# Performance work log

Measured on AMD Instinct MI355X. Metric: run time of the kernel, lower is better.

## Reference

```python
import jax, jax.numpy as jnp
import numpy as np

E, H, I, T, K = 8, 2048, 768, 1024, 2


def setup_inputs() -> dict:
    key = jax.random.key(0)
    k1, k2, k3, k4, k5 = jax.random.split(key, 5)
    hidden_states = jax.random.normal(k1, (T, H), jnp.float32)
    routing_weights = jax.random.uniform(k2, (T, K), jnp.float32)
    selected_experts = jax.random.randint(k3, (T, K), 0, E, jnp.int32)
    gate_up_proj = jax.random.normal(k4, (E, H, 2 * I), jnp.float32) * 0.02
    down_proj = jax.random.normal(k5, (E, I, H), jnp.float32) * 0.02
    return {
        "hidden_states": hidden_states,
        "routing_weights": routing_weights,
        "gate_up_proj": gate_up_proj,
        "down_proj": down_proj,
        "selected_experts": selected_experts,
    }


def _grouped_gemm(x, w, expert_ids):
    # x: [N, k], w: [E, k, d], expert_ids: [N] (sorted by expert).
    # Dense-masked grouped GEMM: accumulate each expert's masked matmul.
    n = x.shape[0]
    acc0 = jnp.zeros((n, w.shape[-1]), x.dtype)

    def step(acc, ew):
        e, we = ew
        xm = jnp.where((expert_ids == e)[:, None], x, jnp.zeros((), x.dtype))
        return acc + xm @ we, None

    acc, _ = jax.lax.scan(step, acc0, (jnp.arange(w.shape[0]), w))
    return acc


def reference(hidden_states, routing_weights, gate_up_proj, down_proj, selected_experts):
    t, h = hidden_states.shape
    k = selected_experts.shape[1]
    flat = selected_experts.reshape(-1)                     # [T*K]
    sort_idx = jnp.argsort(flat)                            # stable sort by expert id (permute)
    token_idx = sort_idx // k                               # source token per permuted row
    permuted = hidden_states[token_idx]                     # [T*K, H]
    experts_sorted = flat[sort_idx]                         # [T*K]

    fc1 = _grouped_gemm(permuted, gate_up_proj, experts_sorted)   # [T*K, 2I]
    a, b = jnp.split(fc1, 2, axis=-1)
    act = jax.nn.silu(a) * b                                # npu_swiglu
    fc2 = _grouped_gemm(act, down_proj, experts_sorted)     # [T*K, H]

    inv = jnp.argsort(sort_idx)                             # unpermute map (row_ids_map)
    unperm = fc2[inv].reshape(t, k, h)                      # [T, K, H]
    return jnp.einsum('tkh,tk->th', unperm, routing_weights)
```

## Files before the change

kernel.cpp:

```cpp
#include <hip/hip_runtime.h>
#include <math.h>

#define E_  8
#define H_  2048
#define I_  768
#define T_  1024
#define K_  2
#define TK_ 2048
#define GU_ 1536

typedef short  short8 __attribute__((ext_vector_type(8)));
typedef __bf16 bf16x8 __attribute__((ext_vector_type(8)));
typedef float  f32x4  __attribute__((ext_vector_type(4)));

static __device__ __forceinline__ short f2bf(float f) {
  union { float f; unsigned u; } v; v.f = f;
  unsigned r = (v.u + 0x7fffu + ((v.u >> 16) & 1u)) >> 16;
  return (short)r;
}

static __device__ __forceinline__ unsigned pk2bf(float a, float b) {
  unsigned ua = __float_as_uint(a) + 0x8000u;
  unsigned ub = __float_as_uint(b) + 0x8000u;
  return __builtin_amdgcn_perm(ub, ua, 0x07060302u);
}

#define GLOAD_LDS16(g, l)                                                   \
  __builtin_amdgcn_global_load_lds(                                         \
      (const __attribute__((address_space(1))) void*)(g),                   \
      (__attribute__((address_space(3))) void*)(l), 16, 0, 0)

#define MFMA_BF16_16x16x32 __builtin_amdgcn_mfma_f32_16x16x32_bf16

static __device__ __forceinline__ bf16x8 frag_ld(const unsigned short* base,
                                                 int row, int oct) {
  return *(const bf16x8*)(base + row * 64 + ((oct ^ (row & 7)) * 8));
}

static __device__ __forceinline__ bf16x8 bfrag_ld(const unsigned short* base,
                                                  int n, int o) {
  const unsigned short* p = base + n * 68 + o * 8;
  uint2 lo = *(const uint2*)p;
  uint2 hi = *(const uint2*)(p + 4);
  union { uint4 u; bf16x8 v; } c;
  c.u = make_uint4(lo.x, lo.y, hi.x, hi.y);
  return c.v;
}

__global__ __launch_bounds__(256) void prep_kernel(
    const float* __restrict__ X, unsigned short* __restrict__ Xb,
    float* __restrict__ out,
    const int* __restrict__ sel, int* __restrict__ offs,
    int* __restrict__ rows) {
  __shared__ int cnt[E_], cur[E_], loff[E_ + 1];
  if (blockIdx.x < 2048) {
    int i = blockIdx.x * 256 + threadIdx.x;
    float4 v = ((const float4*)X)[i];
    unsigned p0 = pk2bf(v.x, v.y), p1 = pk2bf(v.z, v.w);
    ((uint2*)Xb)[i] = make_uint2(p0, p1);
    ((float4*)out)[i] = make_float4(0.f, 0.f, 0.f, 0.f);
    return;
  }
  int t = threadIdx.x;
  if (t < E_) { cnt[t] = 0; cur[t] = 0; }
  __syncthreads();
  for (int p = t; p < TK_; p += 256) atomicAdd(&cnt[sel[p]], 1);
  __syncthreads();
  if (t == 0) {
    int s = 0;
    for (int e = 0; e < E_; ++e) { loff[e] = s; s += cnt[e]; }
    loff[E_] = s;
  }
  __syncthreads();
  if (t <= E_) offs[t] = loff[t];
  for (int p = t; p < TK_; p += 256) {
    int e = sel[p];
    int pos = loff[e] + atomicAdd(&cur[e], 1);
    rows[pos] = p;
  }
}

__global__ __launch_bounds__(256) void fc1_mfma(
    const unsigned short* __restrict__ Xb, const float* __restrict__ GUP,
    const int* __restrict__ offs, const int* __restrict__ rows,
    unsigned short* __restrict__ act) {
  __shared__ __align__(16) unsigned short As[2][128 * 64];
  __shared__ __align__(16) unsigned short Bs[2][64 * 68];

  int e    = blockIdx.y >> 4;
  int rbeg = offs[e], rend = offs[e + 1];
  int row0 = rbeg + (blockIdx.y & 15) * 128;
  if (row0 >= rend) return;
  int c0 = blockIdx.x * 32;

  int tid = threadIdx.x, lane = tid & 63, w = tid >> 6;
  int rl  = lane >> 3;
  int oct = (lane & 7) ^ rl;

  const unsigned short* agp[4];
#pragma unroll
  for (int i = 0; i < 4; ++i) {
    int arow = row0 + w * 32 + i * 8 + rl;
    int aidx = arow < rend ? arow : rend - 1;
    agp[i] = Xb + (size_t)(rows[aidx] >> 1) * H_ + oct * 8;
  }
  auto issueA = [&](int buf, int k0) {
#pragma unroll
    for (int i = 0; i < 4; ++i)
      GLOAD_LDS16(agp[i] + k0, &As[buf][0] + (w * 32 + i * 8) * 64);
  };

  int kt = tid >> 4, nt = tid & 15;
  int gbase = (nt < 8) ? (c0 + nt * 4) : (I_ + c0 + (nt - 8) * 4);
  const float* gupe = GUP + (size_t)e * H_ * GU_ + gbase;

  float4 vb[4];
  auto loadB = [&](int k0) {
#pragma unroll
    for (int i = 0; i < 4; ++i)
      vb[i] = *(const float4*)(gupe + (size_t)(k0 + kt * 4 + i) * GU_);
  };
  auto writeB = [&](int buf) {
#pragma unroll
    for (int j = 0; j < 4; ++j) {
      int n = nt * 4 + j;
      unsigned u0 = pk2bf(((const float*)&vb[0])[j], ((const float*)&vb[1])[j]);
      unsigned u1 = pk2bf(((const float*)&vb[2])[j], ((const float*)&vb[3])[j]);
      *(uint2*)(&Bs[buf][0] + n * 68 + kt * 4) = make_uint2(u0, u1);
    }
  };

  int m = lane & 15, qf = lane >> 4;
  f32x4 acc[2][4] = {};

  issueA(0, 0);
  loadB(0);
  writeB(0);
  int cur = 0;
  const int niter = H_ / 64;
#pragma unroll 1
  for (int it = 0; it < niter; ++it) {
    __syncthreads();
    if (it + 1 < niter) { issueA(cur ^ 1, (it + 1) * 64); loadB((it + 1) * 64); }
    const unsigned short* a_ = &As[cur][0];
    const unsigned short* b_ = &Bs[cur][0];
#pragma unroll
    for (int kk = 0; kk < 2; ++kk) {
      int o = kk * 4 + qf;
      bf16x8 af0 = frag_ld(a_, w * 32 + m,      o);
      bf16x8 af1 = frag_ld(a_, w * 32 + 16 + m, o);
      bf16x8 b0  = bfrag_ld(b_, m,      o);
      bf16x8 b1  = bfrag_ld(b_, 16 + m, o);
      bf16x8 b2  = bfrag_ld(b_, 32 + m, o);
      bf16x8 b3  = bfrag_ld(b_, 48 + m, o);
      acc[0][0] = MFMA_BF16_16x16x32(af0, b0, acc[0][0], 0, 0, 0);
      acc[0][1] = MFMA_BF16_16x16x32(af0, b1, acc[0][1], 0, 0, 0);
      acc[0][2] = MFMA_BF16_16x16x32(af0, b2, acc[0][2], 0, 0, 0);
      acc[0][3] = MFMA_BF16_16x16x32(af0, b3, acc[0][3], 0, 0, 0);
      acc[1][0] = MFMA_BF16_16x16x32(af1, b0, acc[1][0], 0, 0, 0);
      acc[1][1] = MFMA_BF16_16x16x32(af1, b1, acc[1][1], 0, 0, 0);
      acc[1][2] = MFMA_BF16_16x16x32(af1, b2, acc[1][2], 0, 0, 0);
      acc[1][3] = MFMA_BF16_16x16x32(af1, b3, acc[1][3], 0, 0, 0);
    }
    if (it + 1 < niter) writeB(cur ^ 1);
    cur ^= 1;
  }

#pragma unroll
  for (int mt = 0; mt < 2; ++mt)
#pragma unroll
    for (int g = 0; g < 2; ++g)
#pragma unroll
      for (int r = 0; r < 4; ++r) {
        int prow = row0 + w * 32 + mt * 16 + qf * 4 + r;
        if (prow < rend) {
          float gv = acc[mt][g][r], uv = acc[mt][g + 2][r];
          float a = gv / (1.0f + __expf(-gv)) * uv;
          act[(size_t)prow * I_ + c0 + g * 16 + m] = (unsigned short)f2bf(a);
        }
      }
}

__global__ __launch_bounds__(256) void fc2_mfma(
    const unsigned short* __restrict__ act, const float* __restrict__ DWN,
    const float* __restrict__ RW,
    const int* __restrict__ offs, const int* __restrict__ rows,
    float* __restrict__ out) {
  __shared__ __align__(16) unsigned short As[2][128 * 64];
  __shared__ __align__(16) unsigned short Bs[2][64 * 68];

  int e    = blockIdx.y >> 4;
  int rbeg = offs[e], rend = offs[e + 1];
  int row0 = rbeg + (blockIdx.y & 15) * 128;
  if (row0 >= rend) return;
  int c0 = blockIdx.x * 64;

  int tid = threadIdx.x, lane = tid & 63, w = tid >> 6;
  int rl  = lane >> 3;
  int oct = (lane & 7) ^ rl;

  const unsigned short* agp[4];
#pragma unroll
  for (int i = 0; i < 4; ++i) {
    int arow = row0 + w * 32 + i * 8 + rl;
    int aidx = arow < rend ? arow : rend - 1;
    agp[i] = act + (size_t)aidx * I_ + oct * 8;
  }
  auto issueA = [&](int buf, int k0) {
#pragma unroll
    for (int i = 0; i < 4; ++i)
      GLOAD_LDS16(agp[i] + k0, &As[buf][0] + (w * 32 + i * 8) * 64);
  };

  int kt = tid >> 4, nt = tid & 15;
  const float* dwe = DWN + (size_t)e * I_ * H_ + c0 + nt * 4;

  float4 vb[4];
  auto loadB = [&](int k0) {
#pragma unroll
    for (int i = 0; i < 4; ++i)
      vb[i] = *(const float4*)(dwe + (size_t)(k0 + kt * 4 + i) * H_);
  };
  auto writeB = [&](int buf) {
#pragma unroll
    for (int j = 0; j < 4; ++j) {
      int n = nt * 4 + j;
      unsigned u0 = pk2bf(((const float*)&vb[0])[j], ((const float*)&vb[1])[j]);
      unsigned u1 = pk2bf(((const float*)&vb[2])[j], ((const float*)&vb[3])[j]);
      *(uint2*)(&Bs[buf][0] + n * 68 + kt * 4) = make_uint2(u0, u1);
    }
  };

  int m = lane & 15, qf = lane >> 4;
  f32x4 acc[2][4] = {};

  issueA(0, 0);
  loadB(0);
  writeB(0);
  int cur = 0;
  const int niter = I_ / 64;
#pragma unroll 1
  for (int it = 0; it < niter; ++it) {
    __syncthreads();
    if (it + 1 < niter) { issueA(cur ^ 1, (it + 1) * 64); loadB((it + 1) * 64); }
    const unsigned short* a_ = &As[cur][0];
    const unsigned short* b_ = &Bs[cur][0];
#pragma unroll
    for (int kk = 0; kk < 2; ++kk) {
      int o = kk * 4 + qf;
      bf16x8 af0 = frag_ld(a_, w * 32 + m,      o);
      bf16x8 af1 = frag_ld(a_, w * 32 + 16 + m, o);
      bf16x8 b0  = bfrag_ld(b_, m,      o);
      bf16x8 b1  = bfrag_ld(b_, 16 + m, o);
      bf16x8 b2  = bfrag_ld(b_, 32 + m, o);
      bf16x8 b3  = bfrag_ld(b_, 48 + m, o);
      acc[0][0] = MFMA_BF16_16x16x32(af0, b0, acc[0][0], 0, 0, 0);
      acc[0][1] = MFMA_BF16_16x16x32(af0, b1, acc[0][1], 0, 0, 0);
      acc[0][2] = MFMA_BF16_16x16x32(af0, b2, acc[0][2], 0, 0, 0);
      acc[0][3] = MFMA_BF16_16x16x32(af0, b3, acc[0][3], 0, 0, 0);
      acc[1][0] = MFMA_BF16_16x16x32(af1, b0, acc[1][0], 0, 0, 0);
      acc[1][1] = MFMA_BF16_16x16x32(af1, b1, acc[1][1], 0, 0, 0);
      acc[1][2] = MFMA_BF16_16x16x32(af1, b2, acc[1][2], 0, 0, 0);
      acc[1][3] = MFMA_BF16_16x16x32(af1, b3, acc[1][3], 0, 0, 0);
    }
    if (it + 1 < niter) writeB(cur ^ 1);
    cur ^= 1;
  }

#pragma unroll
  for (int mt = 0; mt < 2; ++mt)
#pragma unroll
    for (int r = 0; r < 4; ++r) {
      int prow = row0 + w * 32 + mt * 16 + qf * 4 + r;
      if (prow < rend) {
        int pair = rows[prow];
        float rw = RW[pair];
        float* orow = out + (size_t)(pair >> 1) * H_ + c0 + m;
#pragma unroll
        for (int ntile = 0; ntile < 4; ++ntile)
          atomicAdd(orow + ntile * 16, rw * acc[mt][ntile][r]);
      }
    }
}

extern "C" void kernel_launch(void* const* d_in, const int* in_sizes, int n_in,
                              void* d_out, int out_size, void* d_ws, size_t ws_size,
                              hipStream_t stream) {
  const float* X   = (const float*)d_in[0];
  const float* RW  = (const float*)d_in[1];
  const float* GUP = (const float*)d_in[2];
  const float* DWN = (const float*)d_in[3];
  const int*   SEL = (const int*)d_in[4];
  float* out = (float*)d_out;

  char* ws = (char*)d_ws;
  int* offs = (int*)ws;
  int* rows = (int*)(ws + 1024);
  unsigned short* Xb  = (unsigned short*)(ws + 16384);
  unsigned short* act = (unsigned short*)(ws + 16384 + 4194304);

  hipLaunchKernelGGL(prep_kernel, dim3(2049), dim3(256), 0, stream,
                     X, Xb, out, SEL, offs, rows);
  hipLaunchKernelGGL(fc1_mfma, dim3(24, 128), dim3(256), 0, stream,
                     Xb, GUP, offs, rows, act);
  hipLaunchKernelGGL(fc2_mfma, dim3(32, 128), dim3(256), 0, stream,
                     act, DWN, RW, offs, rows, out);
}
```

Measured before the change: 252.9 us.

## Halve GEMM N-tile, swizzle B in LDS, raise occupancy in expert MFMA kernels

```diff
diff --git a/kernel.cpp b/kernel.cpp
--- a/kernel.cpp
+++ b/kernel.cpp
@@ -35,16 +35,6 @@
 static __device__ __forceinline__ bf16x8 frag_ld(const unsigned short* base,
                                                  int row, int oct) {
   return *(const bf16x8*)(base + row * 64 + ((oct ^ (row & 7)) * 8));
-}
-
-static __device__ __forceinline__ bf16x8 bfrag_ld(const unsigned short* base,
-                                                  int n, int o) {
-  const unsigned short* p = base + n * 68 + o * 8;
-  uint2 lo = *(const uint2*)p;
-  uint2 hi = *(const uint2*)(p + 4);
-  union { uint4 u; bf16x8 v; } c;
-  c.u = make_uint4(lo.x, lo.y, hi.x, hi.y);
-  return c.v;
 }
 
 __global__ __launch_bounds__(256) void prep_kernel(
@@ -80,18 +70,18 @@
   }
 }
 
-__global__ __launch_bounds__(256) void fc1_mfma(
+__global__ __launch_bounds__(256, 4) void fc1_mfma(
     const unsigned short* __restrict__ Xb, const float* __restrict__ GUP,
     const int* __restrict__ offs, const int* __restrict__ rows,
     unsigned short* __restrict__ act) {
   __shared__ __align__(16) unsigned short As[2][128 * 64];
-  __shared__ __align__(16) unsigned short Bs[2][64 * 68];
+  __shared__ __align__(16) unsigned short Bs[2][32 * 64];
 
   int e    = blockIdx.y >> 4;
   int rbeg = offs[e], rend = offs[e + 1];
   int row0 = rbeg + (blockIdx.y & 15) * 128;
   if (row0 >= rend) return;
-  int c0 = blockIdx.x * 32;
+  int c0 = blockIdx.x * 16;
 
   int tid = threadIdx.x, lane = tid & 63, w = tid >> 6;
   int rl  = lane >> 3;
@@ -110,28 +100,28 @@
       GLOAD_LDS16(agp[i] + k0, &As[buf][0] + (w * 32 + i * 8) * 64);
   };
 
-  int kt = tid >> 4, nt = tid & 15;
-  int gbase = (nt < 8) ? (c0 + nt * 4) : (I_ + c0 + (nt - 8) * 4);
-  const float* gupe = GUP + (size_t)e * H_ * GU_ + gbase;
-
-  float4 vb[4];
+  int q = tid & 7, kt2 = tid >> 3;
+  int gcol = (q < 4) ? (c0 + q * 4) : (I_ + c0 + (q - 4) * 4);
+  const float* gupe = GUP + (size_t)e * H_ * GU_ + gcol;
+
+  float4 vb[2];
   auto loadB = [&](int k0) {
 #pragma unroll
-    for (int i = 0; i < 4; ++i)
-      vb[i] = *(const float4*)(gupe + (size_t)(k0 + kt * 4 + i) * GU_);
+    for (int i = 0; i < 2; ++i)
+      vb[i] = *(const float4*)(gupe + (size_t)(k0 + kt2 * 2 + i) * GU_);
   };
   auto writeB = [&](int buf) {
 #pragma unroll
     for (int j = 0; j < 4; ++j) {
-      int n = nt * 4 + j;
-      unsigned u0 = pk2bf(((const float*)&vb[0])[j], ((const float*)&vb[1])[j]);
-      unsigned u1 = pk2bf(((const float*)&vb[2])[j], ((const float*)&vb[3])[j]);
-      *(uint2*)(&Bs[buf][0] + n * 68 + kt * 4) = make_uint2(u0, u1);
+      int n = q * 4 + j;
+      unsigned u = pk2bf(((const float*)&vb[0])[j], ((const float*)&vb[1])[j]);
+      int sw = (kt2 >> 2) ^ (n & 7);
+      *(unsigned*)(&Bs[buf][0] + n * 64 + sw * 8 + ((kt2 * 2) & 7)) = u;
     }
   };
 
   int m = lane & 15, qf = lane >> 4;
-  f32x4 acc[2][4] = {};
+  f32x4 acc[2][2] = {};
 
   issueA(0, 0);
   loadB(0);
@@ -149,18 +139,12 @@
       int o = kk * 4 + qf;
       bf16x8 af0 = frag_ld(a_, w * 32 + m,      o);
       bf16x8 af1 = frag_ld(a_, w * 32 + 16 + m, o);
-      bf16x8 b0  = bfrag_ld(b_, m,      o);
-      bf16x8 b1  = bfrag_ld(b_, 16 + m, o);
-      bf16x8 b2  = bfrag_ld(b_, 32 + m, o);
-      bf16x8 b3  = bfrag_ld(b_, 48 + m, o);
+      bf16x8 b0  = frag_ld(b_, m,      o);
+      bf16x8 b1  = frag_ld(b_, 16 + m, o);
       acc[0][0] = MFMA_BF16_16x16x32(af0, b0, acc[0][0], 0, 0, 0);
       acc[0][1] = MFMA_BF16_16x16x32(af0, b1, acc[0][1], 0, 0, 0);
-      acc[0][2] = MFMA_BF16_16x16x32(af0, b2, acc[0][2], 0, 0, 0);
-      acc[0][3] = MFMA_BF16_16x16x32(af0, b3, acc[0][3], 0, 0, 0);
       acc[1][0] = MFMA_BF16_16x16x32(af1, b0, acc[1][0], 0, 0, 0);
       acc[1][1] = MFMA_BF16_16x16x32(af1, b1, acc[1][1], 0, 0, 0);
-      acc[1][2] = MFMA_BF16_16x16x32(af1, b2, acc[1][2], 0, 0, 0);
-      acc[1][3] = MFMA_BF16_16x16x32(af1, b3, acc[1][3], 0, 0, 0);
     }
     if (it + 1 < niter) writeB(cur ^ 1);
     cur ^= 1;
@@ -169,31 +153,29 @@
 #pragma unroll
   for (int mt = 0; mt < 2; ++mt)
 #pragma unroll
-    for (int g = 0; g < 2; ++g)
-#pragma unroll
-      for (int r = 0; r < 4; ++r) {
-        int prow = row0 + w * 32 + mt * 16 + qf * 4 + r;
-        if (prow < rend) {
-          float gv = acc[mt][g][r], uv = acc[mt][g + 2][r];
-          float a = gv / (1.0f + __expf(-gv)) * uv;
-          act[(size_t)prow * I_ + c0 + g * 16 + m] = (unsigned short)f2bf(a);
-        }
+    for (int r = 0; r < 4; ++r) {
+      int prow = row0 + w * 32 + mt * 16 + qf * 4 + r;
+      if (prow < rend) {
+        float gv = acc[mt][0][r], uv = acc[mt][1][r];
+        float a = gv / (1.0f + __expf(-gv)) * uv;
+        act[(size_t)prow * I_ + c0 + m] = (unsigned short)f2bf(a);
       }
-}
-
-__global__ __launch_bounds__(256) void fc2_mfma(
+    }
+}
+
+__global__ __launch_bounds__(256, 4) void fc2_mfma(
     const unsigned short* __restrict__ act, const float* __restrict__ DWN,
     const float* __restrict__ RW,
     const int* __restrict__ offs, const int* __restrict__ rows,
     float* __restrict__ out) {
   __shared__ __align__(16) unsigned short As[2][128 * 64];
-  __shared__ __align__(16) unsigned short Bs[2][64 * 68];
+  __shared__ __align__(16) unsigned short Bs[2][32 * 64];
 
   int e    = blockIdx.y >> 4;
   int rbeg = offs[e], rend = offs[e + 1];
   int row0 = rbeg + (blockIdx.y & 15) * 128;
   if (row0 >= rend) return;
-  int c0 = blockIdx.x * 64;
+  int c0 = blockIdx.x * 32;
 
   int tid = threadIdx.x, lane = tid & 63, w = tid >> 6;
   int rl  = lane >> 3;
@@ -212,27 +194,27 @@
       GLOAD_LDS16(agp[i] + k0, &As[buf][0] + (w * 32 + i * 8) * 64);
   };
 
-  int kt = tid >> 4, nt = tid & 15;
-  const float* dwe = DWN + (size_t)e * I_ * H_ + c0 + nt * 4;
-
-  float4 vb[4];
+  int q = tid & 7, kt2 = tid >> 3;
+  const float* dwe = DWN + (size_t)e * I_ * H_ + c0 + q * 4;
+
+  float4 vb[2];
   auto loadB = [&](int k0) {
 #pragma unroll
-    for (int i = 0; i < 4; ++i)
-      vb[i] = *(const float4*)(dwe + (size_t)(k0 + kt * 4 + i) * H_);
+    for (int i = 0; i < 2; ++i)
+      vb[i] = *(const float4*)(dwe + (size_t)(k0 + kt2 * 2 + i) * H_);
   };
   auto writeB = [&](int buf) {
 #pragma unroll
     for (int j = 0; j < 4; ++j) {
-      int n = nt * 4 + j;
-      unsigned u0 = pk2bf(((const float*)&vb[0])[j], ((const float*)&vb[1])[j]);
-      unsigned u1 = pk2bf(((const float*)&vb[2])[j], ((const float*)&vb[3])[j]);
-      *(uint2*)(&Bs[buf][0] + n * 68 + kt * 4) = make_uint2(u0, u1);
+      int n = q * 4 + j;
+      unsigned u = pk2bf(((const float*)&vb[0])[j], ((const float*)&vb[1])[j]);
+      int sw = (kt2 >> 2) ^ (n & 7);
+      *(unsigned*)(&Bs[buf][0] + n * 64 + sw * 8 + ((kt2 * 2) & 7)) = u;
     }
   };
 
   int m = lane & 15, qf = lane >> 4;
-  f32x4 acc[2][4] = {};
+  f32x4 acc[2][2] = {};
 
   issueA(0, 0);
   loadB(0);
@@ -250,18 +232,12 @@
       int o = kk * 4 + qf;
       bf16x8 af0 = frag_ld(a_, w * 32 + m,      o);
       bf16x8 af1 = frag_ld(a_, w * 32 + 16 + m, o);
-      bf16x8 b0  = bfrag_ld(b_, m,      o);
-      bf16x8 b1  = bfrag_ld(b_, 16 + m, o);
-      bf16x8 b2  = bfrag_ld(b_, 32 + m, o);
-      bf16x8 b3  = bfrag_ld(b_, 48 + m, o);
+      bf16x8 b0  = frag_ld(b_, m,      o);
+      bf16x8 b1  = frag_ld(b_, 16 + m, o);
       acc[0][0] = MFMA_BF16_16x16x32(af0, b0, acc[0][0], 0, 0, 0);
       acc[0][1] = MFMA_BF16_16x16x32(af0, b1, acc[0][1], 0, 0, 0);
-      acc[0][2] = MFMA_BF16_16x16x32(af0, b2, acc[0][2], 0, 0, 0);
-      acc[0][3] = MFMA_BF16_16x16x32(af0, b3, acc[0][3], 0, 0, 0);
       acc[1][0] = MFMA_BF16_16x16x32(af1, b0, acc[1][0], 0, 0, 0);
       acc[1][1] = MFMA_BF16_16x16x32(af1, b1, acc[1][1], 0, 0, 0);
-      acc[1][2] = MFMA_BF16_16x16x32(af1, b2, acc[1][2], 0, 0, 0);
-      acc[1][3] = MFMA_BF16_16x16x32(af1, b3, acc[1][3], 0, 0, 0);
     }
     if (it + 1 < niter) writeB(cur ^ 1);
     cur ^= 1;
@@ -276,9 +252,8 @@
         int pair = rows[prow];
         float rw = RW[pair];
         float* orow = out + (size_t)(pair >> 1) * H_ + c0 + m;
-#pragma unroll
-        for (int ntile = 0; ntile < 4; ++ntile)
-          atomicAdd(orow + ntile * 16, rw * acc[mt][ntile][r]);
+        atomicAdd(orow,      rw * acc[mt][0][r]);
+        atomicAdd(orow + 16, rw * acc[mt][1][r]);
       }
     }
 }
@@ -301,8 +276,8 @@
 
   hipLaunchKernelGGL(prep_kernel, dim3(2049), dim3(256), 0, stream,
                      X, Xb, out, SEL, offs, rows);
-  hipLaunchKernelGGL(fc1_mfma, dim3(24, 128), dim3(256), 0, stream,
+  hipLaunchKernelGGL(fc1_mfma, dim3(48, 128), dim3(256), 0, stream,
                      Xb, GUP, offs, rows, act);
-  hipLaunchKernelGGL(fc2_mfma, dim3(32, 128), dim3(256), 0, stream,
+  hipLaunchKernelGGL(fc2_mfma, dim3(64, 128), dim3(256), 0, stream,
                      act, DWN, RW, offs, rows, out);
 }
```

New measurement: 280.5 us. +10.9%, slower.

## Deepen B prefetch to two stages, swizzle B LDS layout, hand-schedule waits

Applied to the files above, without the earlier changes.

```diff
diff --git a/kernel.cpp b/kernel.cpp
--- a/kernel.cpp
+++ b/kernel.cpp
@@ -9,7 +9,6 @@
 #define TK_ 2048
 #define GU_ 1536
 
-typedef short  short8 __attribute__((ext_vector_type(8)));
 typedef __bf16 bf16x8 __attribute__((ext_vector_type(8)));
 typedef float  f32x4  __attribute__((ext_vector_type(4)));
 
@@ -37,15 +36,41 @@
   return *(const bf16x8*)(base + row * 64 + ((oct ^ (row & 7)) * 8));
 }
 
-static __device__ __forceinline__ bf16x8 bfrag_ld(const unsigned short* base,
-                                                  int n, int o) {
-  const unsigned short* p = base + n * 68 + o * 8;
-  uint2 lo = *(const uint2*)p;
-  uint2 hi = *(const uint2*)(p + 4);
-  union { uint4 u; bf16x8 v; } c;
-  c.u = make_uint4(lo.x, lo.y, hi.x, hi.y);
-  return c.v;
-}
+#define STEP(IT, VC, VN)                                                    \
+  do {                                                                      \
+    asm volatile("s_waitcnt vmcnt(4)" ::: "memory");                        \
+    __builtin_amdgcn_s_barrier();                                           \
+    __builtin_amdgcn_sched_barrier(0);                                      \
+    int k1_ = ((IT) + 1 < niter ? (IT) + 1 : niter - 1) * 64;               \
+    int k2_ = ((IT) + 2 < niter ? (IT) + 2 : niter - 1) * 64;               \
+    issueA(cur ^ 1, k1_);                                                   \
+    __builtin_amdgcn_sched_barrier(0);                                      \
+    loadB(VN, k2_);                                                         \
+    const unsigned short* a_ = &As[cur][0];                                 \
+    const unsigned short* b_ = &Bs[cur][0];                                 \
+    _Pragma("unroll")                                                       \
+    for (int kk = 0; kk < 2; ++kk) {                                        \
+      int o = kk * 4 + qf;                                                  \
+      bf16x8 af0 = frag_ld(a_, w * 32 + m,      o);                         \
+      bf16x8 af1 = frag_ld(a_, w * 32 + 16 + m, o);                         \
+      bf16x8 b0  = frag_ld(b_, m,      o);                                  \
+      bf16x8 b1  = frag_ld(b_, 16 + m, o);                                  \
+      bf16x8 b2  = frag_ld(b_, 32 + m, o);                                  \
+      bf16x8 b3  = frag_ld(b_, 48 + m, o);                                  \
+      acc[0][0] = MFMA_BF16_16x16x32(af0, b0, acc[0][0], 0, 0, 0);          \
+      acc[0][1] = MFMA_BF16_16x16x32(af0, b1, acc[0][1], 0, 0, 0);          \
+      acc[0][2] = MFMA_BF16_16x16x32(af0, b2, acc[0][2], 0, 0, 0);          \
+      acc[0][3] = MFMA_BF16_16x16x32(af0, b3, acc[0][3], 0, 0, 0);          \
+      acc[1][0] = MFMA_BF16_16x16x32(af1, b0, acc[1][0], 0, 0, 0);          \
+      acc[1][1] = MFMA_BF16_16x16x32(af1, b1, acc[1][1], 0, 0, 0);          \
+      acc[1][2] = MFMA_BF16_16x16x32(af1, b2, acc[1][2], 0, 0, 0);          \
+      acc[1][3] = MFMA_BF16_16x16x32(af1, b3, acc[1][3], 0, 0, 0);          \
+    }                                                                       \
+    writeB(cur ^ 1, VC);                                                    \
+    asm volatile("s_waitcnt lgkmcnt(0)" ::: "memory");                      \
+    __builtin_amdgcn_sched_barrier(0);                                      \
+    cur ^= 1;                                                               \
+  } while (0)
 
 __global__ __launch_bounds__(256) void prep_kernel(
     const float* __restrict__ X, unsigned short* __restrict__ Xb,
@@ -80,12 +105,12 @@
   }
 }
 
-__global__ __launch_bounds__(256) void fc1_mfma(
+__global__ __launch_bounds__(256, 3) void fc1_mfma(
     const unsigned short* __restrict__ Xb, const float* __restrict__ GUP,
     const int* __restrict__ offs, const int* __restrict__ rows,
     unsigned short* __restrict__ act) {
   __shared__ __align__(16) unsigned short As[2][128 * 64];
-  __shared__ __align__(16) unsigned short Bs[2][64 * 68];
+  __shared__ __align__(16) unsigned short Bs[2][64 * 64];
 
   int e    = blockIdx.y >> 4;
   int rbeg = offs[e], rend = offs[e + 1];
@@ -114,56 +139,41 @@
   int gbase = (nt < 8) ? (c0 + nt * 4) : (I_ + c0 + (nt - 8) * 4);
   const float* gupe = GUP + (size_t)e * H_ * GU_ + gbase;
 
-  float4 vb[4];
-  auto loadB = [&](int k0) {
+  auto loadB = [&](float4 (&vb)[4], int k0) {
 #pragma unroll
     for (int i = 0; i < 4; ++i)
       vb[i] = *(const float4*)(gupe + (size_t)(k0 + kt * 4 + i) * GU_);
   };
-  auto writeB = [&](int buf) {
+  auto writeB = [&](int buf, const float4 (&vb)[4]) {
 #pragma unroll
     for (int j = 0; j < 4; ++j) {
       int n = nt * 4 + j;
       unsigned u0 = pk2bf(((const float*)&vb[0])[j], ((const float*)&vb[1])[j]);
       unsigned u1 = pk2bf(((const float*)&vb[2])[j], ((const float*)&vb[3])[j]);
-      *(uint2*)(&Bs[buf][0] + n * 68 + kt * 4) = make_uint2(u0, u1);
+      int phys = (kt >> 1) ^ (n & 7);
+      *(uint2*)(&Bs[buf][0] + n * 64 + phys * 8 + (kt & 1) * 4) =
+          make_uint2(u0, u1);
     }
   };
 
   int m = lane & 15, qf = lane >> 4;
   f32x4 acc[2][4] = {};
+  float4 vbA[4], vbB[4];
 
   issueA(0, 0);
-  loadB(0);
-  writeB(0);
+  __builtin_amdgcn_sched_barrier(0);
+  loadB(vbB, 0);
+  writeB(0, vbB);
+  loadB(vbA, 64);
+  asm volatile("s_waitcnt lgkmcnt(0)" ::: "memory");
+  __builtin_amdgcn_sched_barrier(0);
+
+  const int niter = H_ / 64;
   int cur = 0;
-  const int niter = H_ / 64;
 #pragma unroll 1
-  for (int it = 0; it < niter; ++it) {
-    __syncthreads();
-    if (it + 1 < niter) { issueA(cur ^ 1, (it + 1) * 64); loadB((it + 1) * 64); }
-    const unsigned short* a_ = &As[cur][0];
-    const unsigned short* b_ = &Bs[cur][0];
-#pragma unroll
-    for (int kk = 0; kk < 2; ++kk) {
-      int o = kk * 4 + qf;
-      bf16x8 af0 = frag_ld(a_, w * 32 + m,      o);
-      bf16x8 af1 = frag_ld(a_, w * 32 + 16 + m, o);
-      bf16x8 b0  = bfrag_ld(b_, m,      o);
-      bf16x8 b1  = bfrag_ld(b_, 16 + m, o);
-      bf16x8 b2  = bfrag_ld(b_, 32 + m, o);
-      bf16x8 b3  = bfrag_ld(b_, 48 + m, o);
-      acc[0][0] = MFMA_BF16_16x16x32(af0, b0, acc[0][0], 0, 0, 0);
-      acc[0][1] = MFMA_BF16_16x16x32(af0, b1, acc[0][1], 0, 0, 0);
-      acc[0][2] = MFMA_BF16_16x16x32(af0, b2, acc[0][2], 0, 0, 0);
-      acc[0][3] = MFMA_BF16_16x16x32(af0, b3, acc[0][3], 0, 0, 0);
-      acc[1][0] = MFMA_BF16_16x16x32(af1, b0, acc[1][0], 0, 0, 0);
-      acc[1][1] = MFMA_BF16_16x16x32(af1, b1, acc[1][1], 0, 0, 0);
-      acc[1][2] = MFMA_BF16_16x16x32(af1, b2, acc[1][2], 0, 0, 0);
-      acc[1][3] = MFMA_BF16_16x16x32(af1, b3, acc[1][3], 0, 0, 0);
-    }
-    if (it + 1 < niter) writeB(cur ^ 1);
-    cur ^= 1;
+  for (int it = 0; it < niter; it += 2) {
+    STEP(it,     vbA, vbB);
+    STEP(it + 1, vbB, vbA);
   }
 
 #pragma unroll
@@ -181,13 +191,13 @@
       }
 }
 
-__global__ __launch_bounds__(256) void fc2_mfma(
+__global__ __launch_bounds__(256, 3) void fc2_mfma(
     const unsigned short* __restrict__ act, const float* __restrict__ DWN,
     const float* __restrict__ RW,
     const int* __restrict__ offs, const int* __restrict__ rows,
     float* __restrict__ out) {
   __shared__ __align__(16) unsigned short As[2][128 * 64];
-  __shared__ __align__(16) unsigned short Bs[2][64 * 68];
+  __shared__ __align__(16) unsigned short Bs[2][64 * 64];
 
   int e    = blockIdx.y >> 4;
   int rbeg = offs[e], rend = offs[e + 1];
@@ -215,56 +225,41 @@
   int kt = tid >> 4, nt = tid & 15;
   const float* dwe = DWN + (size_t)e * I_ * H_ + c0 + nt * 4;
 
-  float4 vb[4];
-  auto loadB = [&](int k0) {
+  auto loadB = [&](float4 (&vb)[4], int k0) {
 #pragma unroll
     for (int i = 0; i < 4; ++i)
       vb[i] = *(const float4*)(dwe + (size_t)(k0 + kt * 4 + i) * H_);
   };
-  auto writeB = [&](int buf) {
+  auto writeB = [&](int buf, const float4 (&vb)[4]) {
 #pragma unroll
     for (int j = 0; j < 4; ++j) {
       int n = nt * 4 + j;
       unsigned u0 = pk2bf(((const float*)&vb[0])[j], ((const float*)&vb[1])[j]);
       unsigned u1 = pk2bf(((const float*)&vb[2])[j], ((const float*)&vb[3])[j]);
-      *(uint2*)(&Bs[buf][0] + n * 68 + kt * 4) = make_uint2(u0, u1);
+      int phys = (kt >> 1) ^ (n & 7);
+      *(uint2*)(&Bs[buf][0] + n * 64 + phys * 8 + (kt & 1) * 4) =
+          make_uint2(u0, u1);
     }
   };
 
   int m = lane & 15, qf = lane >> 4;
   f32x4 acc[2][4] = {};
+  float4 vbA[4], vbB[4];
 
   issueA(0, 0);
-  loadB(0);
-  writeB(0);
+  __builtin_amdgcn_sched_barrier(0);
+  loadB(vbB, 0);
+  writeB(0, vbB);
+  loadB(vbA, 64);
+  asm volatile("s_waitcnt lgkmcnt(0)" ::: "memory");
+  __builtin_amdgcn_sched_barrier(0);
+
+  const int niter = I_ / 64;
   int cur = 0;
-  const int niter = I_ / 64;
 #pragma unroll 1
-  for (int it = 0; it < niter; ++it) {
-    __syncthreads();
-    if (it + 1 < niter) { issueA(cur ^ 1, (it + 1) * 64); loadB((it + 1) * 64); }
-    const unsigned short* a_ = &As[cur][0];
-    const unsigned short* b_ = &Bs[cur][0];
-#pragma unroll
-    for (int kk = 0; kk < 2; ++kk) {
-      int o = kk * 4 + qf;
-      bf16x8 af0 = frag_ld(a_, w * 32 + m,      o);
-      bf16x8 af1 = frag_ld(a_, w * 32 + 16 + m, o);
-      bf16x8 b0  = bfrag_ld(b_, m,      o);
-      bf16x8 b1  = bfrag_ld(b_, 16 + m, o);
-      bf16x8 b2  = bfrag_ld(b_, 32 + m, o);
-      bf16x8 b3  = bfrag_ld(b_, 48 + m, o);
-      acc[0][0] = MFMA_BF16_16x16x32(af0, b0, acc[0][0], 0, 0, 0);
-      acc[0][1] = MFMA_BF16_16x16x32(af0, b1, acc[0][1], 0, 0, 0);
-      acc[0][2] = MFMA_BF16_16x16x32(af0, b2, acc[0][2], 0, 0, 0);
-      acc[0][3] = MFMA_BF16_16x16x32(af0, b3, acc[0][3], 0, 0, 0);
-      acc[1][0] = MFMA_BF16_16x16x32(af1, b0, acc[1][0], 0, 0, 0);
-      acc[1][1] = MFMA_BF16_16x16x32(af1, b1, acc[1][1], 0, 0, 0);
-      acc[1][2] = MFMA_BF16_16x16x32(af1, b2, acc[1][2], 0, 0, 0);
-      acc[1][3] = MFMA_BF16_16x16x32(af1, b3, acc[1][3], 0, 0, 0);
-    }
-    if (it + 1 < niter) writeB(cur ^ 1);
-    cur ^= 1;
+  for (int it = 0; it < niter; it += 2) {
+    STEP(it,     vbA, vbB);
+    STEP(it + 1, vbB, vbA);
   }
 
 #pragma unroll
```

New measurement: 253.8 us. No clear change (+0.4%).
